# Kernel optimization log

Hardware: AMD Instinct MI355X
Metric: run time of the kernel (lower is better)

Reference implementation:

```python
import jax, jax.numpy as jnp
import numpy as np

B, T, ENC, DEC, A = 64, 2048, 1024, 1024, 512


def setup_inputs() -> dict:
    key = jax.random.key(0)
    k1, k2, k3, k4, k5 = jax.random.split(key, 5)
    return {
        "h_j": jax.random.normal(k1, (B, T, ENC), dtype=jnp.float32),
        "s_t": jax.random.normal(k2, (B, DEC), dtype=jnp.float32),
        "U_w": jax.random.normal(k3, (ENC, A), dtype=jnp.float32) * (ENC ** -0.5),
        "W_w": jax.random.normal(k4, (DEC, A), dtype=jnp.float32) * (DEC ** -0.5),
        "V_w": jax.random.normal(k5, (A, 1), dtype=jnp.float32) * (A ** -0.5),
    }


def reference(h_j, s_t, U_w, W_w, V_w):
    # f1: [B, T, A] ; f2: [B, 1, A]
    f1 = jnp.einsum("bte,ea->bta", h_j, U_w)
    f2 = (s_t @ W_w)[:, None, :]
    # additive score e_t: [B, T, 1]
    e_t = jnp.tanh(f1 + f2) @ V_w
    a_t = jax.nn.softmax(e_t, axis=1)            # softmax over sequence axis
    c_t = jnp.sum(a_t * h_j, axis=1, keepdims=True)  # [B, 1, ENC]
    return (c_t, a_t)
```

## Files before the change

### kernel.cpp

```cpp
#include <hip/hip_runtime.h>
#include <hip/hip_bf16.h>
#include <stdint.h>

#define B_   64
#define T_   2048
#define ENC_ 1024
#define DEC_ 1024
#define A_   512
#define M_   (B_ * T_)

#define BK   64
#define CH   64
#define NCH  (M_ / CH)
#define CPB  (T_ / CH)
#define NT   (ENC_ / BK)

typedef __bf16 bf16x8 __attribute__((ext_vector_type(8)));
typedef float  f32x4  __attribute__((ext_vector_type(4)));
typedef unsigned short u16;
typedef u16 u16x8 __attribute__((ext_vector_type(8)));

__device__ __forceinline__ float fast_tanh(float x) {
    float ax = fabsf(x);
    float e  = __expf(-2.0f * ax);
    float t  = (1.0f - e) / (1.0f + e);
    return copysignf(t, x);
}

__global__ __launch_bounds__(256) void k_transpose_U(
        const float* __restrict__ U, u16* __restrict__ Ut) {
    __shared__ float tl[64][65];
    const int k0 = blockIdx.x * 64;
    const int n0 = blockIdx.y * 64;
    const int tr = threadIdx.x >> 6;
    const int tc = threadIdx.x & 63;
#pragma unroll
    for (int i = 0; i < 16; ++i) {
        int r = i * 4 + tr;
        tl[r][tc] = U[(size_t)(k0 + r) * A_ + n0 + tc];
    }
    __syncthreads();
#pragma unroll
    for (int i = 0; i < 16; ++i) {
        int nn = i * 4 + tr;
        __bf16 v = (__bf16)tl[tc][nn];
        Ut[(size_t)(n0 + nn) * ENC_ + k0 + tc] = *(u16*)&v;
    }
}

__global__ __launch_bounds__(256) void k_f2(
        const float* __restrict__ s, const float* __restrict__ W,
        float* __restrict__ f2) {
    int b = blockIdx.x;
    int a0 = threadIdx.x;
    const float* srow = s + (size_t)b * DEC_;
    float acc0 = 0.f, acc1 = 0.f;
    for (int e = 0; e < DEC_; ++e) {
        float sv = srow[e];
        acc0 = fmaf(sv, W[(size_t)e * A_ + a0],       acc0);
        acc1 = fmaf(sv, W[(size_t)e * A_ + a0 + 256], acc1);
    }
    f2[(size_t)b * A_ + a0]       = acc0;
    f2[(size_t)b * A_ + a0 + 256] = acc1;
}

__global__ __launch_bounds__(512, 4) void k_gemm_fused(
        const float* __restrict__ h, const u16* __restrict__ Ut,
        const float* __restrict__ f2, const float* __restrict__ V,
        float* __restrict__ e_full, float* __restrict__ mpart,
        float* __restrict__ spart, float* __restrict__ opart) {
    __shared__ u16 Alds[2][CH * BK];
    __shared__ u16 Blds[A_ * BK];
    float* ered = (float*)&Alds[0][0];
    float* wlds = ered + 512;

    const int tid  = threadIdx.x;
    const int lane = tid & 63;
    const int wid  = tid >> 6;
    const int lr   = lane & 15;
    const int g    = lane >> 4;
    const int sw   = (lr & 7) << 3;

    const int d      = blockIdx.x;
    const int gchunk = (d & 7) * 256 + (d >> 3);
    const int brow   = gchunk * CH;
    const int b      = gchunk >> 5;
    const int chunk  = gchunk & 31;

    f32x4 acc[4][4] = {};
    f32x4 ar[2];

    const int arow = tid >> 3;
    const int acol = (tid & 7) * 8;
    auto loadA = [&](int kt) {
        const float* srcA = h + (size_t)(brow + arow) * ENC_ + kt * BK + acol;
        ar[0] = *(const f32x4*)srcA;
        ar[1] = *(const f32x4*)(srcA + 4);
    };
    auto writeA = [&](int buf) {
        u16x8 w;
#pragma unroll
        for (int j = 0; j < 4; ++j) {
            __bf16 lo = (__bf16)ar[0][j], hi = (__bf16)ar[1][j];
            w[j]     = *(u16*)&lo;
            w[j + 4] = *(u16*)&hi;
        }
        *(u16x8*)&Alds[buf][(tid * 8) ^ ((arow & 7) << 3)] = w;
    };
    auto stageB = [&](int kt) {
#pragma unroll
        for (int it = 0; it < 8; ++it) {
            int G  = it * 512 + tid;
            int n  = G >> 3;
            int kc = ((G & 7) ^ (n & 7)) << 3;
            const u16* src = Ut + (size_t)n * ENC_ + kt * BK + kc;
            u16* dst = &Blds[(size_t)(it * 512 + wid * 64) * 8];
            __builtin_amdgcn_global_load_lds(
                (const __attribute__((address_space(1))) void*)src,
                (__attribute__((address_space(3))) void*)dst, 16, 0, 0);
        }
    };
    auto compute = [&](int cur) {
#pragma unroll
        for (int kk = 0; kk < 2; ++kk) {
            bf16x8 af[4], bfr[4];
#pragma unroll
            for (int mf = 0; mf < 4; ++mf)
                af[mf] = *(const bf16x8*)&Alds[cur][
                    (((mf * 16 + lr) * 64) + kk * 32 + g * 8) ^ sw];
#pragma unroll
            for (int nf = 0; nf < 4; ++nf)
                bfr[nf] = *(const bf16x8*)&Blds[
                    (((wid * 64 + nf * 16 + lr) * 64) + kk * 32 + g * 8) ^ sw];
#pragma unroll
            for (int mf = 0; mf < 4; ++mf)
#pragma unroll
                for (int nf = 0; nf < 4; ++nf)
                    acc[mf][nf] = __builtin_amdgcn_mfma_f32_16x16x32_bf16(
                        af[mf], bfr[nf], acc[mf][nf], 0, 0, 0);
        }
    };

    loadA(0);
    writeA(0);
    stageB(0);
    __syncthreads();

    for (int kt = 0; kt < NT; ++kt) {
        const int cur = kt & 1;
        if (kt + 1 < NT) loadA(kt + 1);
        compute(cur);
        if (kt + 1 < NT) {
            writeA(cur ^ 1);
            __syncthreads();
            stageB(kt + 1);
            __syncthreads();
        }
    }

    float vv[4], ff[4];
#pragma unroll
    for (int nf = 0; nf < 4; ++nf) {
        int n = wid * 64 + nf * 16 + lr;
        vv[nf] = V[n];
        ff[nf] = f2[(size_t)b * A_ + n];
    }
#pragma unroll
    for (int mf = 0; mf < 4; ++mf) {
        float sums[4];
#pragma unroll
        for (int i = 0; i < 4; ++i) {
            float sv = 0.f;
#pragma unroll
            for (int nf = 0; nf < 4; ++nf) {
                float x = acc[mf][nf][i] + ff[nf];
                sv = fmaf(fast_tanh(x), vv[nf], sv);
            }
#pragma unroll
            for (int mm = 1; mm < 16; mm <<= 1)
                sv += __shfl_xor(sv, mm, 64);
            sums[i] = sv;
        }
        if (lr == 0) {
#pragma unroll
            for (int i = 0; i < 4; ++i)
                ered[wid * 64 + mf * 16 + g * 4 + i] = sums[i];
        }
    }
    __syncthreads();

    if (tid < 64) {
        float er = 0.f;
#pragma unroll
        for (int w = 0; w < 8; ++w) er += ered[w * 64 + tid];
        float mb = er;
#pragma unroll
        for (int mm = 1; mm < 64; mm <<= 1)
            mb = fmaxf(mb, __shfl_xor(mb, mm, 64));
        float wr_ = __expf(er - mb);
        float sb = wr_;
#pragma unroll
        for (int mm = 1; mm < 64; mm <<= 1)
            sb += __shfl_xor(sb, mm, 64);
        wlds[tid] = wr_;
        e_full[(size_t)b * T_ + chunk * CH + tid] = er;
        if (tid == 0) { mpart[gchunk] = mb; spart[gchunk] = sb; }
    }
    __syncthreads();

    const int c2 = tid * 2;
    float o0 = 0.f, o1 = 0.f;
#pragma unroll 8
    for (int r = 0; r < CH; ++r) {
        float w = wlds[r];
        float2 hv = *(const float2*)(h + (size_t)(brow + r) * ENC_ + c2);
        o0 = fmaf(w, hv.x, o0);
        o1 = fmaf(w, hv.y, o1);
    }
    float* op = opart + (size_t)gchunk * ENC_ + c2;
    op[0] = o0; op[1] = o1;
}

__global__ __launch_bounds__(256) void k_ctx_reduce(
        const float* __restrict__ mpart, const float* __restrict__ spart,
        const float* __restrict__ opart, float* __restrict__ c_out,
        float* __restrict__ mg_g, float* __restrict__ sg_g) {
    const int b = blockIdx.x, tid = threadIdx.x;
    __shared__ float esc[CPB];
    __shared__ float mgS, sgS;

    if (tid < CPB) {
        float mr = mpart[b * CPB + tid];
        float sr = spart[b * CPB + tid];
        float mg = mr;
#pragma unroll
        for (int mm = 1; mm < 32; mm <<= 1)
            mg = fmaxf(mg, __shfl_xor(mg, mm, 32));
        float e = __expf(mr - mg);
        esc[tid] = e;
        float S = sr * e;
#pragma unroll
        for (int mm = 1; mm < 32; mm <<= 1)
            S += __shfl_xor(S, mm, 32);
        if (tid == 0) { mgS = mg; sgS = S; mg_g[b] = mg; sg_g[b] = S; }
    }
    __syncthreads();
    float inv = 1.0f / sgS;
    int c = tid * 4;
    f32x4 av = {0.f, 0.f, 0.f, 0.f};
    for (int r = 0; r < CPB; ++r) {
        f32x4 ov = *(const f32x4*)&opart[((size_t)(b * CPB + r)) * ENC_ + c];
        float e = esc[r];
        av[0] = fmaf(e, ov[0], av[0]); av[1] = fmaf(e, ov[1], av[1]);
        av[2] = fmaf(e, ov[2], av[2]); av[3] = fmaf(e, ov[3], av[3]);
    }
    av[0] *= inv; av[1] *= inv; av[2] *= inv; av[3] *= inv;
    *(f32x4*)&c_out[(size_t)b * ENC_ + c] = av;
}

__global__ __launch_bounds__(256) void k_a_final(
        const float* __restrict__ e_full, const float* __restrict__ mg_g,
        const float* __restrict__ sg_g, float* __restrict__ a_out) {
    int idx = blockIdx.x * 256 + threadIdx.x;
    int b = idx >> 11;
    a_out[idx] = __expf(e_full[idx] - mg_g[b]) / sg_g[b];
}

extern "C" void kernel_launch(void* const* d_in, const int* in_sizes, int n_in,
                              void* d_out, int out_size, void* d_ws, size_t ws_size,
                              hipStream_t stream) {
    const float* h = (const float*)d_in[0];
    const float* s = (const float*)d_in[1];
    const float* U = (const float*)d_in[2];
    const float* W = (const float*)d_in[3];
    const float* V = (const float*)d_in[4];

    float* out   = (float*)d_out;
    float* c_out = out;
    float* a_out = out + 64 * 1024;

    char* ws = (char*)d_ws;
    u16*   Ut = (u16*)ws;
    float* f2 = (float*)(ws + (1 << 20));
    float* e_full = (float*)(ws + 0x120000);
    float* mpart  = (float*)(ws + 0x1A0000);
    float* spart  = (float*)(ws + 0x1A2000);
    float* mg_g   = (float*)(ws + 0x1A4000);
    float* sg_g   = (float*)(ws + 0x1A4100);
    float* opart  = (float*)(ws + 0x200000);

    dim3 gt(ENC_ / 64, A_ / 64);
    k_transpose_U<<<gt, 256, 0, stream>>>(U, Ut);
    k_f2<<<64, 256, 0, stream>>>(s, W, f2);

    k_gemm_fused<<<NCH, 512, 0, stream>>>(h, Ut, f2, V,
                                          e_full, mpart, spart, opart);
    k_ctx_reduce<<<64, 256, 0, stream>>>(mpart, spart, opart,
                                         c_out, mg_g, sg_g);
    k_a_final<<<M_ / 256, 256, 0, stream>>>(e_full, mg_g, sg_g, a_out);
}
```

Measured before the change: 313.6 us.

## Pre-pack U into MFMA fragment layout and load B directly to registers

Replaces the U transpose with a packing kernel that writes bf16 weights in the exact per-lane MFMA fragment order. The GEMM then loads B fragments straight from global memory (L2-resident, 1 MB) into registers each k-step, removing the 64 KB B LDS buffer and one barrier per iteration. Dropping the B tile from LDS may let more blocks fit per CU. The cost is that every block re-reads B from L2, with no LDS reuse across the M fragments. There is also no prefetch, so load latency may be exposed. An extra barrier is added before the epilogue reuses LDS.

After: 306.6 us. 1.02x faster.

```diff
diff --git a/kernel.cpp b/kernel.cpp
--- a/kernel.cpp
+++ b/kernel.cpp
@@ -27,25 +27,20 @@
     return copysignf(t, x);
 }
 
-__global__ __launch_bounds__(256) void k_transpose_U(
-        const float* __restrict__ U, u16* __restrict__ Ut) {
-    __shared__ float tl[64][65];
-    const int k0 = blockIdx.x * 64;
-    const int n0 = blockIdx.y * 64;
-    const int tr = threadIdx.x >> 6;
-    const int tc = threadIdx.x & 63;
-#pragma unroll
-    for (int i = 0; i < 16; ++i) {
-        int r = i * 4 + tr;
-        tl[r][tc] = U[(size_t)(k0 + r) * A_ + n0 + tc];
-    }
-    __syncthreads();
-#pragma unroll
-    for (int i = 0; i < 16; ++i) {
-        int nn = i * 4 + tr;
-        __bf16 v = (__bf16)tl[tc][nn];
-        Ut[(size_t)(n0 + nn) * ENC_ + k0 + tc] = *(u16*)&v;
-    }
+__global__ __launch_bounds__(256) void k_pack_B(
+        const float* __restrict__ U, u16* __restrict__ Bp) {
+    int c = blockIdx.x * 256 + threadIdx.x;
+    int n   = c & 511;
+    int gg  = (c >> 9) & 3;
+    int ks2 = c >> 11;
+    int kbase = ks2 * 32 + gg * 8;
+    u16x8 w;
+#pragma unroll
+    for (int j = 0; j < 8; ++j) {
+        __bf16 v = (__bf16)U[(size_t)(kbase + j) * A_ + n];
+        w[j] = *(u16*)&v;
+    }
+    *(u16x8*)(Bp + (size_t)c * 8) = w;
 }
 
 __global__ __launch_bounds__(256) void k_f2(
@@ -65,12 +60,11 @@
 }
 
 __global__ __launch_bounds__(512, 4) void k_gemm_fused(
-        const float* __restrict__ h, const u16* __restrict__ Ut,
+        const float* __restrict__ h, const u16* __restrict__ Bp,
         const float* __restrict__ f2, const float* __restrict__ V,
         float* __restrict__ e_full, float* __restrict__ mpart,
         float* __restrict__ spart, float* __restrict__ opart) {
     __shared__ u16 Alds[2][CH * BK];
-    __shared__ u16 Blds[A_ * BK];
     float* ered = (float*)&Alds[0][0];
     float* wlds = ered + 512;
 
@@ -107,53 +101,43 @@
         }
         *(u16x8*)&Alds[buf][(tid * 8) ^ ((arow & 7) << 3)] = w;
     };
-    auto stageB = [&](int kt) {
-#pragma unroll
-        for (int it = 0; it < 8; ++it) {
-            int G  = it * 512 + tid;
-            int n  = G >> 3;
-            int kc = ((G & 7) ^ (n & 7)) << 3;
-            const u16* src = Ut + (size_t)n * ENC_ + kt * BK + kc;
-            u16* dst = &Blds[(size_t)(it * 512 + wid * 64) * 8];
-            __builtin_amdgcn_global_load_lds(
-                (const __attribute__((address_space(1))) void*)src,
-                (__attribute__((address_space(3))) void*)dst, 16, 0, 0);
-        }
-    };
-    auto compute = [&](int cur) {
-#pragma unroll
-        for (int kk = 0; kk < 2; ++kk) {
-            bf16x8 af[4], bfr[4];
-#pragma unroll
-            for (int mf = 0; mf < 4; ++mf)
-                af[mf] = *(const bf16x8*)&Alds[cur][
-                    (((mf * 16 + lr) * 64) + kk * 32 + g * 8) ^ sw];
+    const u16* const bbase = Bp + ((size_t)g * 512 + wid * 64 + lr) * 8;
+    auto loadB = [&](int kt, bf16x8 (&b0)[4], bf16x8 (&b1)[4]) {
+        const u16* p0 = bbase + (size_t)(kt * 2)     * 4 * 512 * 8;
+        const u16* p1 = bbase + (size_t)(kt * 2 + 1) * 4 * 512 * 8;
+#pragma unroll
+        for (int nf = 0; nf < 4; ++nf) {
+            b0[nf] = *(const bf16x8*)(p0 + nf * 16 * 8);
+            b1[nf] = *(const bf16x8*)(p1 + nf * 16 * 8);
+        }
+    };
+    auto computeK = [&](int cur, int kk, bf16x8 (&bfr)[4]) {
+        bf16x8 af[4];
+#pragma unroll
+        for (int mf = 0; mf < 4; ++mf)
+            af[mf] = *(const bf16x8*)&Alds[cur][
+                (((mf * 16 + lr) * 64) + kk * 32 + g * 8) ^ sw];
+#pragma unroll
+        for (int mf = 0; mf < 4; ++mf)
 #pragma unroll
             for (int nf = 0; nf < 4; ++nf)
-                bfr[nf] = *(const bf16x8*)&Blds[
-                    (((wid * 64 + nf * 16 + lr) * 64) + kk * 32 + g * 8) ^ sw];
-#pragma unroll
-            for (int mf = 0; mf < 4; ++mf)
-#pragma unroll
-                for (int nf = 0; nf < 4; ++nf)
-                    acc[mf][nf] = __builtin_amdgcn_mfma_f32_16x16x32_bf16(
-                        af[mf], bfr[nf], acc[mf][nf], 0, 0, 0);
-        }
+                acc[mf][nf] = __builtin_amdgcn_mfma_f32_16x16x32_bf16(
+                    af[mf], bfr[nf], acc[mf][nf], 0, 0, 0);
     };
 
     loadA(0);
     writeA(0);
-    stageB(0);
     __syncthreads();
 
     for (int kt = 0; kt < NT; ++kt) {
         const int cur = kt & 1;
+        bf16x8 b0[4], b1[4];
+        loadB(kt, b0, b1);
         if (kt + 1 < NT) loadA(kt + 1);
-        compute(cur);
+        computeK(cur, 0, b0);
+        computeK(cur, 1, b1);
         if (kt + 1 < NT) {
             writeA(cur ^ 1);
-            __syncthreads();
-            stageB(kt + 1);
             __syncthreads();
         }
     }
@@ -165,6 +149,7 @@
         vv[nf] = V[n];
         ff[nf] = f2[(size_t)b * A_ + n];
     }
+    __syncthreads();
 #pragma unroll
     for (int mf = 0; mf < 4; ++mf) {
         float sums[4];
@@ -280,7 +265,7 @@
     float* a_out = out + 64 * 1024;
 
     char* ws = (char*)d_ws;
-    u16*   Ut = (u16*)ws;
+    u16*   Bp = (u16*)ws;
     float* f2 = (float*)(ws + (1 << 20));
     float* e_full = (float*)(ws + 0x120000);
     float* mpart  = (float*)(ws + 0x1A0000);
@@ -289,11 +274,10 @@
     float* sg_g   = (float*)(ws + 0x1A4100);
     float* opart  = (float*)(ws + 0x200000);
 
-    dim3 gt(ENC_ / 64, A_ / 64);
-    k_transpose_U<<<gt, 256, 0, stream>>>(U, Ut);
+    k_pack_B<<<256, 256, 0, stream>>>(U, Bp);
     k_f2<<<64, 256, 0, stream>>>(s, W, f2);
 
-    k_gemm_fused<<<NCH, 512, 0, stream>>>(h, Ut, f2, V,
+    k_gemm_fused<<<NCH, 512, 0, stream>>>(h, Bp, f2, V,
                                           e_full, mpart, spart, opart);
     k_ctx_reduce<<<64, 256, 0, stream>>>(mpart, spart, opart,
                                          c_out, mg_g, sg_g);
```
